# Kernel tuning notes

Hardware: AMD Instinct MI355X
Metric: run time of the kernel (lower is better)

Reference implementation:

```python
import jax, jax.numpy as jnp
import numpy as np

T_VALUES = (4.0, 16.0, 64.0, 256.0)
EPS = 1e-05


def setup_inputs() -> dict:
    key = jax.random.key(0)
    k1, = jax.random.split(key, 1)
    B, F, T = 32, 128, 2000
    x = jax.random.uniform(k1, (B, F, T), dtype=jnp.float32)
    # learned log-parameters, initialized exactly like the torch module
    log_alpha = jnp.full((F,), jnp.log(0.8), dtype=jnp.float32)
    log_delta = jnp.full((F,), jnp.log(10.0), dtype=jnp.float32)
    log_r = jnp.full((F,), jnp.log(0.25), dtype=jnp.float32)
    return {"x": x, "log_alpha": log_alpha, "log_delta": log_delta, "log_r": log_r}


def _mrpcen(x, log_alpha, log_delta, log_r):
    # x: (B, F, T)
    t = jnp.asarray(T_VALUES, dtype=x.dtype)                      # (n_t,)
    s = (jnp.sqrt(1.0 + 4.0 * t ** 2) - 1.0) / (2.0 * t ** 2)     # (n_t,)
    s = s[:, None, None]                                          # (n_t,1,1)

    n_t = len(T_VALUES)
    B, F, T = x.shape
    xt = jnp.moveaxis(x, -1, 0)                                   # (T, B, F)
    m0 = jnp.broadcast_to(xt[0], (n_t, B, F))                     # (n_t, B, F)

    def step(m, x_frame):
        m_new = (1.0 - s) * m + s * x_frame                        # (n_t,B,F)
        return m_new, m_new

    _, ms = jax.lax.scan(step, m0, xt[1:])                        # (T-1, n_t, B, F)
    M = jnp.concatenate([m0[None], ms], axis=0)                   # (T, n_t, B, F)
    M = jnp.moveaxis(M, 0, -1)                                    # (n_t, B, F, T)

    alpha = jnp.exp(log_alpha)[:, None]                           # (F,1)
    delta = jnp.exp(log_delta)[:, None]                           # (F,1)
    r = jnp.exp(log_r)[:, None]                                   # (F,1)

    eps = jnp.asarray(EPS, dtype=x.dtype)
    smooth = jnp.exp(-alpha * (jnp.log(eps) + jnp.log1p(M / eps)))  # (n_t,B,F,T)
    pcen = (x[None] * smooth + delta) ** r - delta ** r             # (n_t,B,F,T)
    return jnp.transpose(pcen, (1, 0, 2, 3))                        # (B,n_t,F,T)


def reference(x, log_alpha, log_delta, log_r):
    return _mrpcen(x, log_alpha, log_delta, log_r)
```

## Files before the change

kernel.cpp:

```cpp
#include <hip/hip_runtime.h>
#include <math.h>


#define NT      4
#define TLEN    2000
#define FDIM    128
#define CHUNK   32
#define LSTRIDE 33
#define ROWPAD  (64 * LSTRIDE)
#define WAVES_PER_BLOCK 2

__global__ __launch_bounds__(128) void mrpcen_kernel(
    const float* __restrict__ x,
    const float* __restrict__ log_alpha,
    const float* __restrict__ log_delta,
    const float* __restrict__ log_r,
    float* __restrict__ out,
    int rows)
{
    __shared__ float xs[WAVES_PER_BLOCK][ROWPAD];
    __shared__ float Ms[WAVES_PER_BLOCK][ROWPAD];

    const int w    = threadIdx.x >> 6;
    const int lane = threadIdx.x & 63;
    const int row  = blockIdx.x * WAVES_PER_BLOCK + w;
    if (row >= rows) return;
    const int b = row >> 7;
    const int f = row & (FDIM - 1);

    const float4* xg4 = (const float4*)(x + (size_t)row * TLEN);
    for (int q = lane; q < TLEN / 4; q += 64) {
        float4 v = xg4[q];
        int p0   = q * 4;
        int bi   = (p0 >> 5) * LSTRIDE + (p0 & 31);
        xs[w][bi + 0] = v.x; xs[w][bi + 1] = v.y;
        xs[w][bi + 2] = v.z; xs[w][bi + 3] = v.w;
    }
    __syncthreads();

    float xr[CHUNK];
#pragma unroll
    for (int j = 0; j < CHUNK; ++j)
        xr[j] = xs[w][lane * LSTRIDE + j];

    const float alpha = __expf(log_alpha[f]);
    const float delta = __expf(log_delta[f]);
    const float rr    = __expf(log_r[f]);
    const float dr    = __expf(rr * __logf(delta));
    const float eps   = 1e-5f;

    const float tvals[NT] = {4.f, 16.f, 64.f, 256.f};

#pragma unroll 1
    for (int ti = 0; ti < NT; ++ti) {
        const float t  = tvals[ti];
        const float s  = (sqrtf(1.f + 4.f * t * t) - 1.f) / (2.f * t * t);
        const float cs = 1.f - s;

        float A = 1.f, B = 0.f;
#pragma unroll
        for (int j = 0; j < CHUNK; ++j) {
            int pos  = lane * CHUNK + j;
            float a  = (pos < TLEN) ? cs : 1.0f;
            float bb = (pos < TLEN) ? s * xr[j] : 0.0f;
            if (pos == 0) { a = 0.0f; bb = xr[j]; }
            B = fmaf(a, B, bb);
            A = a * A;
        }

#pragma unroll
        for (int off = 1; off < 64; off <<= 1) {
            float Ap = __shfl_up(A, off, 64);
            float Bp = __shfl_up(B, off, 64);
            if (lane >= off) {
                B = fmaf(A, Bp, B);
                A = A * Ap;
            }
        }
        float m = __shfl_up(B, 1, 64);

#pragma unroll
        for (int j = 0; j < CHUNK; ++j) {
            int pos  = lane * CHUNK + j;
            float a  = (pos < TLEN) ? cs : 1.0f;
            float bb = (pos < TLEN) ? s * xr[j] : 0.0f;
            if (pos == 0) { a = 0.0f; bb = xr[j]; }
            m = fmaf(a, m, bb);
            if (pos < TLEN) Ms[w][lane * LSTRIDE + j] = m;
        }
        __syncthreads();

        float* gout = out + ((size_t)(b * NT + ti) * FDIM + f) * TLEN;
        for (int pos = lane; pos < TLEN; pos += 64) {
            int idx      = (pos >> 5) * LSTRIDE + (pos & 31);
            float xv     = xs[w][idx];
            float Mv     = Ms[w][idx];
            float smooth = __expf(-alpha * __logf(eps + Mv));
            float v      = fmaf(xv, smooth, delta);
            gout[pos]    = __expf(rr * __logf(v)) - dr;
        }
        __syncthreads();
    }
}

extern "C" void kernel_launch(void* const* d_in, const int* in_sizes, int n_in,
                              void* d_out, int out_size, void* d_ws, size_t ws_size,
                              hipStream_t stream) {
    const float* x  = (const float*)d_in[0];
    const float* la = (const float*)d_in[1];
    const float* ld = (const float*)d_in[2];
    const float* lr = (const float*)d_in[3];
    float* out = (float*)d_out;

    const int rows   = in_sizes[0] / TLEN;
    const int blocks = (rows + WAVES_PER_BLOCK - 1) / WAVES_PER_BLOCK;
    hipLaunchKernelGGL(mrpcen_kernel, dim3(blocks), dim3(128), 0, stream,
                       x, la, ld, lr, out, rows);
}
```

Baseline: 207.3 us.

## Fuse PCEN math into scan, reuse single LDS stage buffer, 4 waves per block

Computes the smoothing and power-law output directly in registers during the second scan pass, then writes the results into one shared staging buffer that is reused for coalesced global stores. This replaces the separate Ms buffer and the later reload pass. The per-lane chunk decay product is now computed in closed form from powers of (1-s) instead of being multiplied up in the loop. Blocks grow to 4 waves, and out-of-range rows are masked instead of returning early so barriers stay safe. Overwriting the x data in the stage buffer is correct only because xr already holds the values in registers, and the extra transcendentals inside the unrolled loop raise register pressure.

New measurement: 177.4 us. -14.4%, faster.

```diff
diff --git a/kernel.cpp b/kernel.cpp
--- a/kernel.cpp
+++ b/kernel.cpp
@@ -8,9 +8,9 @@
 #define CHUNK   32
 #define LSTRIDE 33
 #define ROWPAD  (64 * LSTRIDE)
-#define WAVES_PER_BLOCK 2
+#define WPB     4
 
-__global__ __launch_bounds__(128) void mrpcen_kernel(
+__global__ __launch_bounds__(256) void mrpcen_kernel(
     const float* __restrict__ x,
     const float* __restrict__ log_alpha,
     const float* __restrict__ log_delta,
@@ -18,34 +18,36 @@
     float* __restrict__ out,
     int rows)
 {
-    __shared__ float xs[WAVES_PER_BLOCK][ROWPAD];
-    __shared__ float Ms[WAVES_PER_BLOCK][ROWPAD];
+    __shared__ float stage[WPB][ROWPAD];
 
     const int w    = threadIdx.x >> 6;
     const int lane = threadIdx.x & 63;
-    const int row  = blockIdx.x * WAVES_PER_BLOCK + w;
-    if (row >= rows) return;
+    const int row  = blockIdx.x * WPB + w;
+    const bool live = (row < rows);
     const int b = row >> 7;
     const int f = row & (FDIM - 1);
 
-    const float4* xg4 = (const float4*)(x + (size_t)row * TLEN);
-    for (int q = lane; q < TLEN / 4; q += 64) {
-        float4 v = xg4[q];
-        int p0   = q * 4;
-        int bi   = (p0 >> 5) * LSTRIDE + (p0 & 31);
-        xs[w][bi + 0] = v.x; xs[w][bi + 1] = v.y;
-        xs[w][bi + 2] = v.z; xs[w][bi + 3] = v.w;
+    if (live) {
+        const float4* xg4 = (const float4*)(x + (size_t)row * TLEN);
+        for (int q = lane; q < TLEN / 4; q += 64) {
+            float4 v = xg4[q];
+            int p0 = q * 4;
+            int bi = (p0 >> 5) * LSTRIDE + (p0 & 31);
+            stage[w][bi + 0] = v.x; stage[w][bi + 1] = v.y;
+            stage[w][bi + 2] = v.z; stage[w][bi + 3] = v.w;
+        }
     }
     __syncthreads();
 
     float xr[CHUNK];
 #pragma unroll
     for (int j = 0; j < CHUNK; ++j)
-        xr[j] = xs[w][lane * LSTRIDE + j];
+        xr[j] = stage[w][lane * LSTRIDE + j];
 
-    const float alpha = __expf(log_alpha[f]);
-    const float delta = __expf(log_delta[f]);
-    const float rr    = __expf(log_r[f]);
+    const int ff = live ? f : 0;
+    const float alpha = __expf(log_alpha[ff]);
+    const float delta = __expf(log_delta[ff]);
+    const float rr    = __expf(log_r[ff]);
     const float dr    = __expf(rr * __logf(delta));
     const float eps   = 1e-5f;
 
@@ -57,7 +59,11 @@
         const float s  = (sqrtf(1.f + 4.f * t * t) - 1.f) / (2.f * t * t);
         const float cs = 1.f - s;
 
-        float A = 1.f, B = 0.f;
+        float c2  = cs * cs, c4 = c2 * c2, c8 = c4 * c4;
+        float c16 = c8 * c8, c32 = c16 * c16;
+        float A = (lane == 0) ? 0.f : (lane < 62) ? c32 : (lane == 62) ? c16 : 1.f;
+
+        float B = 0.f;
 #pragma unroll
         for (int j = 0; j < CHUNK; ++j) {
             int pos  = lane * CHUNK + j;
@@ -65,7 +71,6 @@
             float bb = (pos < TLEN) ? s * xr[j] : 0.0f;
             if (pos == 0) { a = 0.0f; bb = xr[j]; }
             B = fmaf(a, B, bb);
-            A = a * A;
         }
 
 #pragma unroll
@@ -86,18 +91,20 @@
             float bb = (pos < TLEN) ? s * xr[j] : 0.0f;
             if (pos == 0) { a = 0.0f; bb = xr[j]; }
             m = fmaf(a, m, bb);
-            if (pos < TLEN) Ms[w][lane * LSTRIDE + j] = m;
+            if (pos < TLEN) {
+                float smooth = __expf(-alpha * __logf(eps + m));
+                float v      = fmaf(xr[j], smooth, delta);
+                stage[w][lane * LSTRIDE + j] = __expf(rr * __logf(v)) - dr;
+            }
         }
         __syncthreads();
 
-        float* gout = out + ((size_t)(b * NT + ti) * FDIM + f) * TLEN;
-        for (int pos = lane; pos < TLEN; pos += 64) {
-            int idx      = (pos >> 5) * LSTRIDE + (pos & 31);
-            float xv     = xs[w][idx];
-            float Mv     = Ms[w][idx];
-            float smooth = __expf(-alpha * __logf(eps + Mv));
-            float v      = fmaf(xv, smooth, delta);
-            gout[pos]    = __expf(rr * __logf(v)) - dr;
+        if (live) {
+            float* gout = out + ((size_t)(b * NT + ti) * FDIM + f) * TLEN;
+            for (int pos = lane; pos < TLEN; pos += 64) {
+                int idx = (pos >> 5) * LSTRIDE + (pos & 31);
+                gout[pos] = stage[w][idx];
+            }
         }
         __syncthreads();
     }
@@ -113,7 +120,7 @@
     float* out = (float*)d_out;
 
     const int rows   = in_sizes[0] / TLEN;
-    const int blocks = (rows + WAVES_PER_BLOCK - 1) / WAVES_PER_BLOCK;
-    hipLaunchKernelGGL(mrpcen_kernel, dim3(blocks), dim3(128), 0, stream,
+    const int blocks = (rows + WPB - 1) / WPB;
+    hipLaunchKernelGGL(mrpcen_kernel, dim3(blocks), dim3(256), 0, stream,
                        x, la, ld, lr, out, rows);
 }
```
